# Kernel optimization log

Hardware: AMD Instinct MI355X
Metric: run time of the kernel (lower is better)

Reference implementation:

```python
import jax, jax.numpy as jnp
import numpy as np

EMBED = 1024
HEAD = 1024

def setup_inputs() -> dict:
    key = jax.random.key(0)
    k0, k1, k2, k3 = jax.random.split(key, 4)
    x = jax.random.normal(k0, (4, 4096, EMBED), dtype=jnp.float32)
    s = 1.0 / np.sqrt(EMBED)
    Wq = jax.random.normal(k1, (EMBED, HEAD), dtype=jnp.float32) * s
    Wk = jax.random.normal(k2, (EMBED, HEAD), dtype=jnp.float32) * s
    Wv = jax.random.normal(k3, (EMBED, HEAD), dtype=jnp.float32) * s
    return {"x": x, "Wq": Wq, "Wk": Wk, "Wv": Wv}

def reference(x, Wq, Wk, Wv):
    # x: [b, s, e]; projections: [b, s, h]
    Q = jnp.einsum('bse,eh->bsh', x, Wq)
    K = jnp.einsum('bse,eh->bsh', x, Wk)
    V = jnp.einsum('bse,eh->bsh', x, Wv)
    scale = 1.0 / jnp.sqrt(jnp.asarray(HEAD, dtype=Q.dtype))
    scores = jnp.einsum('bqh,bkh->bqk', Q, K) * scale  # [b, s, s]
    seq_len = x.shape[1]
    causal = jnp.tril(jnp.ones((seq_len, seq_len), dtype=bool))
    scores = jnp.where(causal[None, :, :], scores, -jnp.inf)
    weights = jax.nn.softmax(scores, axis=-1)
    out = jnp.einsum('bqk,bkh->bqh', weights, V)
    return out
```

## Files before the change

kernel.cpp:

```cpp
#include <hip/hip_runtime.h>

typedef float  f32x4 __attribute__((ext_vector_type(4)));
typedef short  s16x8 __attribute__((ext_vector_type(8)));
typedef unsigned short u16;
typedef unsigned short u16x8 __attribute__((ext_vector_type(8)));

#define MFMA __builtin_amdgcn_mfma_f32_16x16x32_bf16

#define SEQ 4096
#define DIM 1024
#define NB  4

__device__ inline u16 f2bf(float f) {
  union { float f; unsigned u; } v; v.f = f;
  unsigned r = v.u + 0x7FFFu + ((v.u >> 16) & 1u);
  return (u16)(r >> 16);
}

__global__ __launch_bounds__(256) void xcvt(const float* __restrict__ X, u16* __restrict__ X16) {
  size_t i = ((size_t)blockIdx.x * 256 + threadIdx.x) * 8;
  f32x4 a = *(const f32x4*)(X + i);
  f32x4 b = *(const f32x4*)(X + i + 4);
  u16x8 p;
  p[0] = f2bf(a[0]); p[1] = f2bf(a[1]); p[2] = f2bf(a[2]); p[3] = f2bf(a[3]);
  p[4] = f2bf(b[0]); p[5] = f2bf(b[1]); p[6] = f2bf(b[2]); p[7] = f2bf(b[3]);
  *(u16x8*)(X16 + i) = p;
}

__global__ __launch_bounds__(256) void wcvt(const float* __restrict__ W, u16* __restrict__ Wt) {
  __shared__ float tile[32][33];
  int t = threadIdx.x, tx = t & 31, ty = t >> 5;
  int e0 = blockIdx.y * 32, h0 = blockIdx.x * 32;
#pragma unroll
  for (int i = 0; i < 4; ++i)
    tile[ty + i * 8][tx] = W[(size_t)(e0 + ty + i * 8) * DIM + h0 + tx];
  __syncthreads();
#pragma unroll
  for (int i = 0; i < 4; ++i)
    Wt[(size_t)(h0 + ty + i * 8) * DIM + e0 + tx] = f2bf(tile[tx][ty + i * 8]);
}

__global__ __launch_bounds__(256) void vtrans(const u16* __restrict__ V, u16* __restrict__ Vt) {
  __shared__ u16 tile[32][34];
  int t = threadIdx.x, tx = t & 31, ty = t >> 5;
  int b = blockIdx.z;
  int s0 = blockIdx.x * 32, h0 = blockIdx.y * 32;
  const u16* Vb = V + (size_t)b * SEQ * DIM;
  u16* Vtb = Vt + (size_t)b * DIM * SEQ;
#pragma unroll
  for (int i = 0; i < 4; ++i)
    tile[ty + i * 8][tx] = Vb[(size_t)(s0 + ty + i * 8) * DIM + h0 + tx];
  __syncthreads();
#pragma unroll
  for (int i = 0; i < 4; ++i)
    Vtb[(size_t)(h0 + ty + i * 8) * SEQ + s0 + tx] = tile[tx][ty + i * 8];
}

__global__ __launch_bounds__(256, 2) void gemm_xw(const u16* __restrict__ X16,
                                                  const u16* __restrict__ Wt,
                                                  u16* __restrict__ C) {
  const int K = DIM, N = DIM;
  __shared__ u16 As[128 * 40];
  __shared__ u16 Bs[128 * 40];
  int m0 = blockIdx.y * 128, n0 = blockIdx.x * 128;
  int t = threadIdx.x, lane = t & 63, w = t >> 6;
  int wr = w >> 1, wc = w & 1;
  int l16 = lane & 15, lh = lane >> 4;
  f32x4 acc[4][4] = {};
  for (int kb = 0; kb < K; kb += 32) {
    __syncthreads();
#pragma unroll
    for (int i = 0; i < 2; ++i) {
      int c = t + i * 256, row = c >> 2, cc = c & 3;
      *(u16x8*)&As[row * 40 + cc * 8] = *(const u16x8*)(X16 + (size_t)(m0 + row) * K + kb + cc * 8);
      *(u16x8*)&Bs[row * 40 + cc * 8] = *(const u16x8*)(Wt  + (size_t)(n0 + row) * K + kb + cc * 8);
    }
    __syncthreads();
    s16x8 af[4], bfr[4];
#pragma unroll
    for (int mt = 0; mt < 4; ++mt)
      af[mt] = *(const s16x8*)&As[(wr * 64 + mt * 16 + l16) * 40 + lh * 8];
#pragma unroll
    for (int nt = 0; nt < 4; ++nt)
      bfr[nt] = *(const s16x8*)&Bs[(wc * 64 + nt * 16 + l16) * 40 + lh * 8];
#pragma unroll
    for (int mt = 0; mt < 4; ++mt)
#pragma unroll
      for (int nt = 0; nt < 4; ++nt)
        acc[mt][nt] = MFMA(af[mt], bfr[nt], acc[mt][nt], 0, 0, 0);
  }
#pragma unroll
  for (int mt = 0; mt < 4; ++mt)
#pragma unroll
    for (int nt = 0; nt < 4; ++nt)
#pragma unroll
      for (int r = 0; r < 4; ++r) {
        int row = m0 + wr * 64 + mt * 16 + lh * 4 + r;
        int col = n0 + wc * 64 + nt * 16 + l16;
        C[(size_t)row * N + col] = f2bf(acc[mt][nt][r]);
      }
}

__global__ __launch_bounds__(512, 2) void attn(const u16* __restrict__ Q,
                                               const u16* __restrict__ Kg,
                                               const u16* __restrict__ Vt,
                                               float* __restrict__ O) {
  __shared__ float Sp[4][128][36];
  __shared__ u16   Pl[32][136];
  __shared__ float alpha_l[32];
  __shared__ float lsum_l[32];

  int bid = blockIdx.x;
  int batch = (bid & 7) >> 1;
  int pi = ((bid >> 3) << 1) | (bid & 1);

  int t = threadIdx.x, lane = t & 63, w = t >> 6;
  int d = w >> 1, kg = w & 1;
  int l16 = lane & 15, lh = lane >> 4;
  int myrow = t >> 4, mycol = t & 15;

  const u16* Qb = Q  + (size_t)batch * SEQ * DIM;
  const u16* Kb = Kg + (size_t)batch * SEQ * DIM;
  const u16* Vb = Vt + (size_t)batch * DIM * SEQ;
  float*     Ob = O  + (size_t)batch * SEQ * DIM;

#pragma unroll
  for (int tile = 0; tile < 2; ++tile) {
    int qt = tile ? (127 - pi) : pi;
    int q0 = qt * 32;
    int nkb = (qt >> 2) + 1;

    s16x8 qf[2][8];
#pragma unroll
    for (int mt = 0; mt < 2; ++mt)
#pragma unroll
      for (int kc = 0; kc < 8; ++kc)
        qf[mt][kc] = *(const s16x8*)(Qb + (size_t)(q0 + mt * 16 + l16) * DIM + d * 256 + kc * 32 + lh * 8);

    f32x4 acc[2][8] = {};
    float m_run = -1e30f, l_run = 0.f;

    for (int kb = 0; kb < nkb; ++kb) {
      int k0 = kb * 128;
      f32x4 sf[2][4] = {};
#pragma unroll
      for (int kc = 0; kc < 8; ++kc)
#pragma unroll
        for (int nt = 0; nt < 4; ++nt) {
          s16x8 kf = *(const s16x8*)(Kb + (size_t)(k0 + kg * 64 + nt * 16 + l16) * DIM + d * 256 + kc * 32 + lh * 8);
          sf[0][nt] = MFMA(qf[0][kc], kf, sf[0][nt], 0, 0, 0);
          sf[1][nt] = MFMA(qf[1][kc], kf, sf[1][nt], 0, 0, 0);
        }
#pragma unroll
      for (int mt = 0; mt < 2; ++mt)
#pragma unroll
        for (int nt = 0; nt < 4; ++nt)
          *(f32x4*)&Sp[d][kg * 64 + nt * 16 + l16][mt * 16 + lh * 4] = sf[mt][nt];
      __syncthreads();

      float s[8], p[8];
#pragma unroll
      for (int j = 0; j < 8; ++j) {
        int c = mycol + 16 * j;
        float v = Sp[0][c][myrow] + Sp[1][c][myrow] + Sp[2][c][myrow] + Sp[3][c][myrow];
        v *= 0.03125f;
        s[j] = (k0 + c > q0 + myrow) ? -1e30f : v;
      }
      float mb = s[0];
#pragma unroll
      for (int j = 1; j < 8; ++j) mb = fmaxf(mb, s[j]);
#pragma unroll
      for (int off = 1; off < 16; off <<= 1) mb = fmaxf(mb, __shfl_xor(mb, off, 16));
      float m_new = fmaxf(m_run, mb);
      float al = __expf(m_run - m_new);
      float lb = 0.f;
#pragma unroll
      for (int j = 0; j < 8; ++j) { p[j] = __expf(s[j] - m_new); lb += p[j]; }
#pragma unroll
      for (int off = 1; off < 16; off <<= 1) lb += __shfl_xor(lb, off, 16);
      l_run = l_run * al + lb;
      m_run = m_new;
#pragma unroll
      for (int j = 0; j < 8; ++j) Pl[myrow][mycol + 16 * j] = f2bf(p[j]);
      if (mycol == 0) alpha_l[myrow] = al;
      __syncthreads();

      float a0[4], a1[4];
#pragma unroll
      for (int r = 0; r < 4; ++r) { a0[r] = alpha_l[lh * 4 + r]; a1[r] = alpha_l[16 + lh * 4 + r]; }
#pragma unroll
      for (int nt = 0; nt < 8; ++nt)
#pragma unroll
        for (int r = 0; r < 4; ++r) { acc[0][nt][r] *= a0[r]; acc[1][nt][r] *= a1[r]; }
      s16x8 pf[2][4];
#pragma unroll
      for (int mt = 0; mt < 2; ++mt)
#pragma unroll
        for (int kc = 0; kc < 4; ++kc)
          pf[mt][kc] = *(const s16x8*)&Pl[mt * 16 + l16][kc * 32 + lh * 8];
#pragma unroll
      for (int kc = 0; kc < 4; ++kc)
#pragma unroll
        for (int nt = 0; nt < 8; ++nt) {
          s16x8 vf = *(const s16x8*)(Vb + (size_t)(w * 128 + nt * 16 + l16) * SEQ + k0 + kc * 32 + lh * 8);
          acc[0][nt] = MFMA(pf[0][kc], vf, acc[0][nt], 0, 0, 0);
          acc[1][nt] = MFMA(pf[1][kc], vf, acc[1][nt], 0, 0, 0);
        }
    }

    if (mycol == 0) lsum_l[myrow] = l_run;
    __syncthreads();
    float li0[4], li1[4];
#pragma unroll
    for (int r = 0; r < 4; ++r) {
      li0[r] = 1.f / lsum_l[lh * 4 + r];
      li1[r] = 1.f / lsum_l[16 + lh * 4 + r];
    }
#pragma unroll
    for (int nt = 0; nt < 8; ++nt)
#pragma unroll
      for (int r = 0; r < 4; ++r) {
        Ob[(size_t)(q0 + lh * 4 + r)      * DIM + w * 128 + nt * 16 + l16] = acc[0][nt][r] * li0[r];
        Ob[(size_t)(q0 + 16 + lh * 4 + r) * DIM + w * 128 + nt * 16 + l16] = acc[1][nt][r] * li1[r];
      }
    __syncthreads();
  }
}

extern "C" void kernel_launch(void* const* d_in, const int* in_sizes, int n_in,
                              void* d_out, int out_size, void* d_ws, size_t ws_size,
                              hipStream_t stream) {
  const float* x  = (const float*)d_in[0];
  const float* Wq = (const float*)d_in[1];
  const float* Wk = (const float*)d_in[2];
  const float* Wv = (const float*)d_in[3];
  float* out = (float*)d_out;

  u16* Wtq = (u16*)d_ws;
  u16* Wtk = Wtq + (size_t)DIM * DIM;
  u16* Wtv = Wtk + (size_t)DIM * DIM;
  u16* X16 = Wtv + (size_t)DIM * DIM;
  u16* Qb  = X16 + (size_t)NB * SEQ * DIM;
  u16* Kb  = Qb  + (size_t)NB * SEQ * DIM;
  u16* Vb  = Kb  + (size_t)NB * SEQ * DIM;
  u16* Vtb = X16;

  xcvt<<<dim3(8192), dim3(256), 0, stream>>>(x, X16);

  wcvt<<<dim3(32, 32), dim3(256), 0, stream>>>(Wq, Wtq);
  wcvt<<<dim3(32, 32), dim3(256), 0, stream>>>(Wk, Wtk);
  wcvt<<<dim3(32, 32), dim3(256), 0, stream>>>(Wv, Wtv);

  gemm_xw<<<dim3(8, 128), dim3(256), 0, stream>>>(X16, Wtq, Qb);
  gemm_xw<<<dim3(8, 128), dim3(256), 0, stream>>>(X16, Wtk, Kb);
  gemm_xw<<<dim3(8, 128), dim3(256), 0, stream>>>(X16, Wtv, Vb);

  vtrans<<<dim3(128, 32, 4), dim3(256), 0, stream>>>(Vb, Vtb);

  attn<<<dim3(256), dim3(512), 0, stream>>>(Qb, Kb, Vtb, out);
}
```

Measured before the change: 813.7 us.

## Launch one query tile per block with zigzag scheduling and bf16 partial scores

Each attention block now handles a single 32-row query tile instead of a balanced pair, doubling the grid to 512 blocks. Heavy tiles are ordered first in a zigzag pattern to even out causal load. The per-split partial score buffer in shared memory is stored as bf16 rather than fp32, halving LDS use so that four blocks per CU can be resident. The cost is lower precision in the partial dot products before the split-sum, plus reliance on the hardware scheduler for load balance.

```diff
diff --git a/kernel.cpp b/kernel.cpp
--- a/kernel.cpp
+++ b/kernel.cpp
@@ -3,6 +3,7 @@
 typedef float  f32x4 __attribute__((ext_vector_type(4)));
 typedef short  s16x8 __attribute__((ext_vector_type(8)));
 typedef unsigned short u16;
+typedef unsigned short u16x4 __attribute__((ext_vector_type(4)));
 typedef unsigned short u16x8 __attribute__((ext_vector_type(8)));
 
 #define MFMA __builtin_amdgcn_mfma_f32_16x16x32_bf16
@@ -15,6 +16,10 @@
   union { float f; unsigned u; } v; v.f = f;
   unsigned r = v.u + 0x7FFFu + ((v.u >> 16) & 1u);
   return (u16)(r >> 16);
+}
+__device__ inline float bf2f(u16 b) {
+  union { unsigned u; float f; } v; v.u = ((unsigned)b) << 16;
+  return v.f;
 }
 
 __global__ __launch_bounds__(256) void xcvt(const float* __restrict__ X, u16* __restrict__ X16) {
@@ -101,18 +106,23 @@
       }
 }
 
-__global__ __launch_bounds__(512, 2) void attn(const u16* __restrict__ Q,
+__global__ __launch_bounds__(512, 4) void attn(const u16* __restrict__ Q,
                                                const u16* __restrict__ Kg,
                                                const u16* __restrict__ Vt,
                                                float* __restrict__ O) {
-  __shared__ float Sp[4][128][36];
+  __shared__ u16   Sp[4][128][36];
   __shared__ u16   Pl[32][136];
   __shared__ float alpha_l[32];
   __shared__ float lsum_l[32];
 
   int bid = blockIdx.x;
-  int batch = (bid & 7) >> 1;
-  int pi = ((bid >> 3) << 1) | (bid & 1);
+  int xcd = bid & 7;
+  int batch = xcd >> 1;
+  int r = bid >> 3;
+  int rz = (r & 1) ? (63 - (r >> 1)) : (r >> 1);
+  int qt = 127 - (2 * rz + (xcd & 1));
+  int q0 = qt * 32;
+  int nkb = (qt >> 2) + 1;
 
   int t = threadIdx.x, lane = t & 63, w = t >> 6;
   int d = w >> 1, kg = w & 1;
@@ -124,107 +134,104 @@
   const u16* Vb = Vt + (size_t)batch * DIM * SEQ;
   float*     Ob = O  + (size_t)batch * SEQ * DIM;
 
-#pragma unroll
-  for (int tile = 0; tile < 2; ++tile) {
-    int qt = tile ? (127 - pi) : pi;
-    int q0 = qt * 32;
-    int nkb = (qt >> 2) + 1;
-
-    s16x8 qf[2][8];
+  s16x8 qf[2][8];
+#pragma unroll
+  for (int mt = 0; mt < 2; ++mt)
+#pragma unroll
+    for (int kc = 0; kc < 8; ++kc)
+      qf[mt][kc] = *(const s16x8*)(Qb + (size_t)(q0 + mt * 16 + l16) * DIM + d * 256 + kc * 32 + lh * 8);
+
+  f32x4 acc[2][8] = {};
+  float m_run = -1e30f, l_run = 0.f;
+
+  for (int kb = 0; kb < nkb; ++kb) {
+    int k0 = kb * 128;
+    f32x4 sf[2][4] = {};
+#pragma unroll
+    for (int kc = 0; kc < 8; ++kc)
+#pragma unroll
+      for (int nt = 0; nt < 4; ++nt) {
+        s16x8 kf = *(const s16x8*)(Kb + (size_t)(k0 + kg * 64 + nt * 16 + l16) * DIM + d * 256 + kc * 32 + lh * 8);
+        sf[0][nt] = MFMA(qf[0][kc], kf, sf[0][nt], 0, 0, 0);
+        sf[1][nt] = MFMA(qf[1][kc], kf, sf[1][nt], 0, 0, 0);
+      }
 #pragma unroll
     for (int mt = 0; mt < 2; ++mt)
 #pragma unroll
-      for (int kc = 0; kc < 8; ++kc)
-        qf[mt][kc] = *(const s16x8*)(Qb + (size_t)(q0 + mt * 16 + l16) * DIM + d * 256 + kc * 32 + lh * 8);
-
-    f32x4 acc[2][8] = {};
-    float m_run = -1e30f, l_run = 0.f;
-
-    for (int kb = 0; kb < nkb; ++kb) {
-      int k0 = kb * 128;
-      f32x4 sf[2][4] = {};
-#pragma unroll
-      for (int kc = 0; kc < 8; ++kc)
-#pragma unroll
-        for (int nt = 0; nt < 4; ++nt) {
-          s16x8 kf = *(const s16x8*)(Kb + (size_t)(k0 + kg * 64 + nt * 16 + l16) * DIM + d * 256 + kc * 32 + lh * 8);
-          sf[0][nt] = MFMA(qf[0][kc], kf, sf[0][nt], 0, 0, 0);
-          sf[1][nt] = MFMA(qf[1][kc], kf, sf[1][nt], 0, 0, 0);
-        }
-#pragma unroll
-      for (int mt = 0; mt < 2; ++mt)
-#pragma unroll
-        for (int nt = 0; nt < 4; ++nt)
-          *(f32x4*)&Sp[d][kg * 64 + nt * 16 + l16][mt * 16 + lh * 4] = sf[mt][nt];
-      __syncthreads();
-
-      float s[8], p[8];
-#pragma unroll
-      for (int j = 0; j < 8; ++j) {
-        int c = mycol + 16 * j;
-        float v = Sp[0][c][myrow] + Sp[1][c][myrow] + Sp[2][c][myrow] + Sp[3][c][myrow];
-        v *= 0.03125f;
-        s[j] = (k0 + c > q0 + myrow) ? -1e30f : v;
-      }
-      float mb = s[0];
-#pragma unroll
-      for (int j = 1; j < 8; ++j) mb = fmaxf(mb, s[j]);
-#pragma unroll
-      for (int off = 1; off < 16; off <<= 1) mb = fmaxf(mb, __shfl_xor(mb, off, 16));
-      float m_new = fmaxf(m_run, mb);
-      float al = __expf(m_run - m_new);
-      float lb = 0.f;
-#pragma unroll
-      for (int j = 0; j < 8; ++j) { p[j] = __expf(s[j] - m_new); lb += p[j]; }
-#pragma unroll
-      for (int off = 1; off < 16; off <<= 1) lb += __shfl_xor(lb, off, 16);
-      l_run = l_run * al + lb;
-      m_run = m_new;
-#pragma unroll
-      for (int j = 0; j < 8; ++j) Pl[myrow][mycol + 16 * j] = f2bf(p[j]);
-      if (mycol == 0) alpha_l[myrow] = al;
-      __syncthreads();
-
-      float a0[4], a1[4];
-#pragma unroll
-      for (int r = 0; r < 4; ++r) { a0[r] = alpha_l[lh * 4 + r]; a1[r] = alpha_l[16 + lh * 4 + r]; }
-#pragma unroll
-      for (int nt = 0; nt < 8; ++nt)
-#pragma unroll
-        for (int r = 0; r < 4; ++r) { acc[0][nt][r] *= a0[r]; acc[1][nt][r] *= a1[r]; }
-      s16x8 pf[2][4];
-#pragma unroll
-      for (int mt = 0; mt < 2; ++mt)
-#pragma unroll
-        for (int kc = 0; kc < 4; ++kc)
-          pf[mt][kc] = *(const s16x8*)&Pl[mt * 16 + l16][kc * 32 + lh * 8];
+      for (int nt = 0; nt < 4; ++nt) {
+        u16x4 pk;
+#pragma unroll
+        for (int rr = 0; rr < 4; ++rr) pk[rr] = f2bf(sf[mt][nt][rr]);
+        *(u16x4*)&Sp[d][kg * 64 + nt * 16 + l16][mt * 16 + lh * 4] = pk;
+      }
+    __syncthreads();
+
+    float s[8], p[8];
+#pragma unroll
+    for (int j = 0; j < 8; ++j) {
+      int c = mycol + 16 * j;
+      float v = bf2f(Sp[0][c][myrow]) + bf2f(Sp[1][c][myrow])
+              + bf2f(Sp[2][c][myrow]) + bf2f(Sp[3][c][myrow]);
+      v *= 0.03125f;
+      s[j] = (k0 + c > q0 + myrow) ? -1e30f : v;
+    }
+    float mb = s[0];
+#pragma unroll
+    for (int j = 1; j < 8; ++j) mb = fmaxf(mb, s[j]);
+#pragma unroll
+    for (int off = 1; off < 16; off <<= 1) mb = fmaxf(mb, __shfl_xor(mb, off, 16));
+    float m_new = fmaxf(m_run, mb);
+    float al = __expf(m_run - m_new);
+    float lb = 0.f;
+#pragma unroll
+    for (int j = 0; j < 8; ++j) { p[j] = __expf(s[j] - m_new); lb += p[j]; }
+#pragma unroll
+    for (int off = 1; off < 16; off <<= 1) lb += __shfl_xor(lb, off, 16);
+    l_run = l_run * al + lb;
+    m_run = m_new;
+#pragma unroll
+    for (int j = 0; j < 8; ++j) Pl[myrow][mycol + 16 * j] = f2bf(p[j]);
+    if (mycol == 0) alpha_l[myrow] = al;
+    __syncthreads();
+
+    float a0[4], a1[4];
+#pragma unroll
+    for (int rr = 0; rr < 4; ++rr) { a0[rr] = alpha_l[lh * 4 + rr]; a1[rr] = alpha_l[16 + lh * 4 + rr]; }
+#pragma unroll
+    for (int nt = 0; nt < 8; ++nt)
+#pragma unroll
+      for (int rr = 0; rr < 4; ++rr) { acc[0][nt][rr] *= a0[rr]; acc[1][nt][rr] *= a1[rr]; }
+    s16x8 pf[2][4];
+#pragma unroll
+    for (int mt = 0; mt < 2; ++mt)
 #pragma unroll
       for (int kc = 0; kc < 4; ++kc)
-#pragma unroll
-        for (int nt = 0; nt < 8; ++nt) {
-          s16x8 vf = *(const s16x8*)(Vb + (size_t)(w * 128 + nt * 16 + l16) * SEQ + k0 + kc * 32 + lh * 8);
-          acc[0][nt] = MFMA(pf[0][kc], vf, acc[0][nt], 0, 0, 0);
-          acc[1][nt] = MFMA(pf[1][kc], vf, acc[1][nt], 0, 0, 0);
-        }
+        pf[mt][kc] = *(const s16x8*)&Pl[mt * 16 + l16][kc * 32 + lh * 8];
+#pragma unroll
+    for (int kc = 0; kc < 4; ++kc)
+#pragma unroll
+      for (int nt = 0; nt < 8; ++nt) {
+        s16x8 vf = *(const s16x8*)(Vb + (size_t)(w * 128 + nt * 16 + l16) * SEQ + k0 + kc * 32 + lh * 8);
+        acc[0][nt] = MFMA(pf[0][kc], vf, acc[0][nt], 0, 0, 0);
+        acc[1][nt] = MFMA(pf[1][kc], vf, acc[1][nt], 0, 0, 0);
+      }
+  }
+
+  if (mycol == 0) lsum_l[myrow] = l_run;
+  __syncthreads();
+  float li0[4], li1[4];
+#pragma unroll
+  for (int rr = 0; rr < 4; ++rr) {
+    li0[rr] = 1.f / lsum_l[lh * 4 + rr];
+    li1[rr] = 1.f / lsum_l[16 + lh * 4 + rr];
+  }
+#pragma unroll
+  for (int nt = 0; nt < 8; ++nt)
+#pragma unroll
+    for (int rr = 0; rr < 4; ++rr) {
+      Ob[(size_t)(q0 + lh * 4 + rr)      * DIM + w * 128 + nt * 16 + l16] = acc[0][nt][rr] * li0[rr];
+      Ob[(size_t)(q0 + 16 + lh * 4 + rr) * DIM + w * 128 + nt * 16 + l16] = acc[1][nt][rr] * li1[rr];
     }
-
-    if (mycol == 0) lsum_l[myrow] = l_run;
-    __syncthreads();
-    float li0[4], li1[4];
-#pragma unroll
-    for (int r = 0; r < 4; ++r) {
-      li0[r] = 1.f / lsum_l[lh * 4 + r];
-      li1[r] = 1.f / lsum_l[16 + lh * 4 + r];
-    }
-#pragma unroll
-    for (int nt = 0; nt < 8; ++nt)
-#pragma unroll
-      for (int r = 0; r < 4; ++r) {
-        Ob[(size_t)(q0 + lh * 4 + r)      * DIM + w * 128 + nt * 16 + l16] = acc[0][nt][r] * li0[r];
-        Ob[(size_t)(q0 + 16 + lh * 4 + r) * DIM + w * 128 + nt * 16 + l16] = acc[1][nt][r] * li1[r];
-      }
-    __syncthreads();
-  }
 }
 
 extern "C" void kernel_launch(void* const* d_in, const int* in_sizes, int n_in,
@@ -257,5 +264,5 @@
 
   vtrans<<<dim3(128, 32, 4), dim3(256), 0, stream>>>(Vb, Vtb);
 
-  attn<<<dim3(256), dim3(512), 0, stream>>>(Qb, Kb, Vtb, out);
-}
+  attn<<<dim3(512), dim3(512), 0, stream>>>(Qb, Kb, Vtb, out);
+}
```

Result: slower. 1.491 ms (+83.2%).
